# Kernel optimization log

Measured on AMD Instinct MI355X. Metric: run time of the kernel, lower is better.

The kernel has to match this reference:

```python
import jax, jax.numpy as jnp
import numpy as np
import math

EPS = 1e-5

def _bn_lrelu(x, g, b, m, v):
    # BatchNorm2d (eval, running stats) + LeakyReLU(0.01)
    inv = jax.lax.rsqrt(v + EPS)
    xn = (x - m[None, :, None, None]) * (g * inv)[None, :, None, None] + b[None, :, None, None]
    return jnp.where(xn >= 0, xn, 0.01 * xn)

def _conv3x3(x, w, b):
    # zero pad 1 on freq (dim2) and time (dim3) (pad_left state is None -> zeros), valid 3x3 conv
    x = jnp.pad(x, ((0, 0), (0, 0), (1, 1), (1, 1)))
    y = jax.lax.conv_general_dilated(x, w, (1, 1), 'VALID',
                                     dimension_numbers=('NCHW', 'OIHW', 'NCHW'))
    return y + b[None, :, None, None]

def _conv1x1(x, w, b):
    return jnp.einsum('bcft,oc->boft', x, w[:, :, 0, 0]) + b[None, :, None, None]

def _blockx3(x, g, b, m, v, w, wb):
    return _conv3x3(_bn_lrelu(x, g, b, m, v), w, wb)

def _mha(x, wqkv, bqkv, wo, bo, n_heads=4, L=64, U=128):
    # banded local attention over time, window = (L back, L fwd), chunked by U
    B, C, F, T = x.shape
    H = n_heads; D = C // H; S = 2 * L
    qkv = _conv1x1(x, wqkv, bqkv)                 # [B,3C,F,T]
    qkv = qkv.transpose(0, 2, 1, 3)               # [B,F,3C,T]
    def split(a):
        return a.reshape(B * F, H, D, T).transpose(0, 1, 3, 2)  # [BF,H,T,D]
    q = split(qkv[:, :, :C])
    k = split(qkv[:, :, C:2 * C])
    v = split(qkv[:, :, 2 * C:])
    Tkv = T + L                                   # kv padded left by L (zero state)
    nC = T // U
    pad_to = nC * U + S                           # pad kv right so every chunk window exists
    kp = jnp.pad(k, ((0, 0), (0, 0), (L, pad_to - Tkv), (0, 0)))
    vp = jnp.pad(v, ((0, 0), (0, 0), (L, pad_to - Tkv), (0, 0)))
    idx = (jnp.arange(nC) * U)[:, None] + jnp.arange(U + S)[None, :]   # [nC, U+S]
    kc = kp[:, :, idx, :]                         # [BF,H,nC,U+S,D]
    vc = vp[:, :, idx, :]
    qc = q.reshape(B * F, H, nC, U, D)
    i = jnp.arange(U)[:, None]; j = jnp.arange(U + S)[None, :]
    band = (j >= i) & (j <= i + S)                # row i sees cols i..i+S (width 1+2L)
    valid = (jnp.arange(nC)[:, None] * U + jnp.arange(U + S)[None, :]) < Tkv
    mask = (band[None, :, :] & valid[:, None, :]).astype(x.dtype)      # [nC,U,U+S]
    scores = jnp.einsum('bhcqd,bhckd->bhcqk', qc, kc) / math.sqrt(D)
    scores = scores * mask - 10000.0 * (1.0 - mask)
    p = jax.nn.softmax(scores, axis=-1)
    o = jnp.einsum('bhcqk,bhckd->bhcqd', p, vc)   # [BF,H,nC,U,D]
    o = o.reshape(B * F, H, T, D).transpose(0, 1, 3, 2).reshape(B, F, C, T).transpose(0, 2, 1, 3)
    return _conv1x1(o, wo, bo)

def setup_inputs() -> dict:
    key = jax.random.key(0)
    ks = jax.random.split(key, 40)
    d = {}
    d['x'] = jax.random.normal(ks[0], (4, 64, 64, 512), dtype=jnp.float32)
    def bn(i, c, pre):
        d[pre + '_g'] = jax.random.normal(ks[i], (c,), jnp.float32) * 0.1 + 1.0
        d[pre + '_b'] = jax.random.normal(ks[i + 1], (c,), jnp.float32) * 0.1
        d[pre + '_m'] = jax.random.normal(ks[i + 2], (c,), jnp.float32) * 0.1
        d[pre + '_v'] = jax.random.uniform(ks[i + 3], (c,), jnp.float32, 0.5, 1.5)
    def conv(i, o, c, kh, kw, pre):
        fan = c * kh * kw
        d[pre + '_w'] = jax.random.normal(ks[i], (o, c, kh, kw), jnp.float32) / math.sqrt(fan)
        d[pre + '_wb'] = jax.random.normal(ks[i + 1], (o,), jnp.float32) * 0.01
    bn(1, 64, 'bd0');  conv(5, 32, 64, 3, 3, 'bd0')
    bn(7, 96, 'bd1');  conv(11, 32, 96, 3, 3, 'bd1')
    bn(13, 128, 'bdo'); conv(17, 64, 128, 3, 3, 'bdo')
    d['qkv_w'] = jax.random.normal(ks[19], (192, 64, 1, 1), jnp.float32) / math.sqrt(64)
    d['qkv_b'] = jax.random.normal(ks[20], (192,), jnp.float32) * 0.01
    d['o_w'] = jax.random.normal(ks[21], (64, 64, 1, 1), jnp.float32) / math.sqrt(64)
    d['o_b'] = jax.random.normal(ks[22], (64,), jnp.float32) * 0.01
    bn(23, 128, 'sao'); conv(27, 64, 128, 1, 1, 'sao')
    return d

def reference(x,
              bd0_g, bd0_b, bd0_m, bd0_v, bd0_w, bd0_wb,
              bd1_g, bd1_b, bd1_m, bd1_v, bd1_w, bd1_wb,
              bdo_g, bdo_b, bdo_m, bdo_v, bdo_w, bdo_wb,
              qkv_w, qkv_b, o_w, o_b,
              sao_g, sao_b, sao_m, sao_v, sao_w, sao_wb):
    # dense conv stack: 64 -> +32 -> +32 -> 64
    a0 = _blockx3(x, bd0_g, bd0_b, bd0_m, bd0_v, bd0_w, bd0_wb)
    x1 = jnp.concatenate([x, a0], axis=1)                 # [B,96,F,T]
    a1 = _blockx3(x1, bd1_g, bd1_b, bd1_m, bd1_v, bd1_w, bd1_wb)
    x2 = jnp.concatenate([x1, a1], axis=1)                # [B,128,F,T]
    y = _blockx3(x2, bdo_g, bdo_b, bdo_m, bdo_v, bdo_w, bdo_wb)  # [B,64,F,T]
    # banded self-attention branch
    att = _mha(y, qkv_w, qkv_b, o_w, o_b)                 # [B,64,F,T]
    z = jnp.concatenate([y, att], axis=1)                 # [B,128,F,T]
    out = _conv1x1(_bn_lrelu(z, sao_g, sao_b, sao_m, sao_v), sao_w, sao_wb)
    return out
```

## Files before the change

### kernel.cpp

```cpp
#include <hip/hip_runtime.h>
#include <hip/hip_bf16.h>

typedef unsigned short u16t;
typedef __attribute__((ext_vector_type(8))) short bfrag;
typedef __attribute__((ext_vector_type(4))) float f32x4;
typedef __attribute__((ext_vector_type(8))) unsigned short uh8;

__device__ __forceinline__ float bfu(u16t u) {
    union { unsigned int i; float f; } c;
    c.i = ((unsigned int)u) << 16;
    return c.f;
}
__device__ __forceinline__ u16t fbf(float f) {
    __hip_bfloat16 h = __float2bfloat16(f);
    return *reinterpret_cast<u16t*>(&h);
}

__global__ __launch_bounds__(256) void prep_x3_k(
    const float* __restrict__ x,
    const float* __restrict__ g0, const float* __restrict__ b0,
    const float* __restrict__ m0, const float* __restrict__ v0,
    const float* __restrict__ g1, const float* __restrict__ b1,
    const float* __restrict__ m1, const float* __restrict__ v1,
    const float* __restrict__ g2, const float* __restrict__ b2,
    const float* __restrict__ m2, const float* __restrict__ v2,
    u16t* __restrict__ xn0, u16t* __restrict__ xn1, u16t* __restrict__ xn2)
{
    constexpr int F = 64, T = 512;
    __shared__ u16t su[64][74];
    __shared__ float ssc[3][64], ssh[3][64];
    const int tid = threadIdx.x;
    const int t0 = blockIdx.x * 64;
    const int f = blockIdx.y, b = blockIdx.z;

    if (tid < 64) {
        int c = tid;
        float s;
        s = g0[c] * rsqrtf(v0[c] + 1e-5f); ssc[0][c] = s; ssh[0][c] = b0[c] - m0[c] * s;
        s = g1[c] * rsqrtf(v1[c] + 1e-5f); ssc[1][c] = s; ssh[1][c] = b1[c] - m1[c] * s;
        s = g2[c] * rsqrtf(v2[c] + 1e-5f); ssc[2][c] = s; ssh[2][c] = b2[c] - m2[c] * s;
    }
#pragma unroll
    for (int p = 0; p < 16; p++) {
        int i = tid + 256 * p;
        int c = i >> 6, t = i & 63;
        su[c][t] = fbf(x[(((long)b * 64 + c) * F + f) * T + t0 + t]);
    }
    __syncthreads();
#pragma unroll
    for (int p = 0; p < 2; p++) {
        int i = tid + 256 * p;
        int t = i >> 3, c8 = i & 7;
        uh8 o0, o1, o2;
#pragma unroll
        for (int j = 0; j < 8; j++) {
            int c = c8 * 8 + j;
            float xv = bfu(su[c][t]);
            float n0 = fmaf(xv, ssc[0][c], ssh[0][c]);
            float n1 = fmaf(xv, ssc[1][c], ssh[1][c]);
            float n2 = fmaf(xv, ssc[2][c], ssh[2][c]);
            o0[j] = fbf(fmaxf(n0, 0.01f * n0));
            o1[j] = fbf(fmaxf(n1, 0.01f * n1));
            o2[j] = fbf(fmaxf(n2, 0.01f * n2));
        }
        long gi = (((long)b * F + f) * T + t0 + t) * 64 + c8 * 8;
        *(uh8*)&xn0[gi] = o0;
        *(uh8*)&xn1[gi] = o1;
        *(uh8*)&xn2[gi] = o2;
    }
}

__global__ __launch_bounds__(256) void prep_w_k(
    const float* __restrict__ w0, const float* __restrict__ w1,
    const float* __restrict__ w2, const float* __restrict__ ow,
    const float* __restrict__ sw, const float* __restrict__ qw,
    u16t* __restrict__ wp)
{
    int idx = blockIdx.x * 256 + threadIdx.x;
    if (idx >= 144384) return;
    if (idx < 119808) {
        int C_IN, C_OUT, e;
        const float* src;
        if (idx < 18432)      { C_IN = 64;  C_OUT = 32; src = w0; e = idx; }
        else if (idx < 46080) { C_IN = 96;  C_OUT = 32; src = w1; e = idx - 18432; }
        else                  { C_IN = 128; C_OUT = 64; src = w2; e = idx - 46080; }
        int NCOT = C_OUT / 16;
        int j  = e & 7;
        int l  = (e >> 3) & 63;
        int r  = e >> 9;
        int ct = r % NCOT;
        int r2 = r / NCOT;
        int kk = r2 % 9;
        int cb = r2 / 9;
        int co  = ct * 16 + (l & 15);
        int kin = cb * 32 + (l >> 4) * 8 + j;
        int kh = kk / 3, kw = kk % 3;
        wp[idx] = fbf(src[((co * C_IN + kin) * 3 + kh) * 3 + kw]);
    } else if (idx < 123904) {
        int e = idx - 119808;
        int ks = e & 31, co = (e >> 5) & 63, kb = e >> 11;
        wp[idx] = fbf(ow[co * 64 + kb * 32 + ks]);
    } else if (idx < 132096) {
        int e = idx - 123904;
        int ks = e & 31, co = (e >> 5) & 63, kb = e >> 11;
        wp[idx] = fbf(sw[co * 128 + kb * 32 + ks]);
    } else {
        int e = idx - 132096;
        int ks = e & 31, co = (e >> 5) % 192, kb = e / 6144;
        wp[idx] = fbf(qw[co * 64 + kb * 32 + ks]);
    }
}

template<int C_IN, int C_OUT, int EPI>
__global__ __launch_bounds__(256) void conv3x3_ff4_k(
    const u16t* __restrict__ s0, const u16t* __restrict__ s1,
    const u16t* __restrict__ s2,
    const u16t* __restrict__ wseg, const float* __restrict__ wb,
    const float* __restrict__ g1, const float* __restrict__ b1,
    const float* __restrict__ m1, const float* __restrict__ v1,
    const float* __restrict__ g2, const float* __restrict__ b2,
    const float* __restrict__ m2, const float* __restrict__ v2,
    int bnoff, u16t* __restrict__ dst1, u16t* __restrict__ dst2)
{
    constexpr int F = 64, T = 512, TT = 64, FF = 4;
    constexpr int NCH  = C_IN / 32;
    constexpr int NCOT = C_OUT / 16;
    constexpr int WT = 9 * NCOT * 64;
    constexpr int XT = 6 * 66 * 4;

    __shared__ __align__(16) u16t s_x[6][66][40];
    __shared__ __align__(16) u16t s_w[WT * 8];

    const int tid = threadIdx.x;
    const int t0 = blockIdx.x * TT;
    const int f0 = blockIdx.y * FF;
    const int b  = blockIdx.z;

    const int l  = tid & 63;
    const int wv = tid >> 6;
    const int lr = l & 15;
    const int lq = l >> 4;

    f32x4 acc[4][NCOT];
#pragma unroll
    for (int i = 0; i < 4; i++)
#pragma unroll
        for (int j = 0; j < NCOT; j++) acc[i][j] = (f32x4){0.f, 0.f, 0.f, 0.f};

    for (int ch = 0; ch < NCH; ch++) {
        if (ch) __syncthreads();

        for (int idx = tid; idx < XT + WT; idx += 256) {
            if (idx < XT) {
                int oct = idx & 3;
                int row = idx >> 2;
                int fr = row / 66;
                int tp = row - fr * 66;
                int fi = f0 + fr - 1;
                int tg = t0 + tp - 1;
                int gc8 = ch * 4 + oct;
                uh8 v = (uh8)0;
                if ((unsigned)fi < (unsigned)F && (unsigned)tg < (unsigned)T) {
                    const u16t* sp; int coff, cw;
                    if (C_IN == 64 || gc8 < 8) { sp = s0; coff = gc8 * 8;        cw = 64; }
                    else if (gc8 < 12)         { sp = s1; coff = (gc8 - 8) * 8;  cw = 32; }
                    else                       { sp = s2; coff = (gc8 - 12) * 8; cw = 32; }
                    v = *(const uh8*)&sp[(((long)b * F + fi) * T + tg) * cw + coff];
                }
                *(uh8*)&s_x[fr][tp][oct * 8] = v;
            } else {
                int w = idx - XT;
                *(uh8*)&s_w[w * 8] = *(const uh8*)&wseg[((long)ch * WT + w) * 8];
            }
        }
        __syncthreads();

#pragma unroll
        for (int kk = 0; kk < 9; kk++) {
            const int kh = kk / 3, kw = kk % 3;
            bfrag A[NCOT];
#pragma unroll
            for (int ct = 0; ct < NCOT; ct++)
                A[ct] = *(const bfrag*)&s_w[((kk * NCOT + ct) * 64 + l) * 8];
#pragma unroll
            for (int ts = 0; ts < 4; ts++) {
                bfrag B = *(const bfrag*)&s_x[wv + kh][ts * 16 + lr + kw][lq * 8];
#pragma unroll
                for (int ct = 0; ct < NCOT; ct++)
                    acc[ts][ct] = __builtin_amdgcn_mfma_f32_16x16x32_bf16(
                        A[ct], B, acc[ts][ct], 0, 0, 0);
            }
        }
    }

    const int f = f0 + wv;
#pragma unroll
    for (int ct = 0; ct < NCOT; ct++) {
        const int co0 = ct * 16 + lq * 4;
        float4 bs = *(const float4*)&wb[co0];
        float sc1[4], sh1[4], sc2[4], sh2[4];
        if (EPI >= 1) {
#pragma unroll
            for (int j = 0; j < 4; j++) {
                int c = bnoff + co0 + j;
                float s = g1[c] * rsqrtf(v1[c] + 1e-5f);
                sc1[j] = s; sh1[j] = b1[c] - m1[c] * s;
            }
        }
        if (EPI == 2) {
#pragma unroll
            for (int j = 0; j < 4; j++) {
                int c = bnoff + co0 + j;
                float s = g2[c] * rsqrtf(v2[c] + 1e-5f);
                sc2[j] = s; sh2[j] = b2[c] - m2[c] * s;
            }
        }
#pragma unroll
        for (int ts = 0; ts < 4; ts++) {
            const int t = t0 + ts * 16 + lr;
            long ob = (((long)b * F + f) * T + t) * C_OUT + co0;
            float a[4];
            a[0] = acc[ts][ct][0] + bs.x;
            a[1] = acc[ts][ct][1] + bs.y;
            a[2] = acc[ts][ct][2] + bs.z;
            a[3] = acc[ts][ct][3] + bs.w;
            if (EPI == 0) {
                ushort4 pk;
                pk.x = fbf(a[0]); pk.y = fbf(a[1]);
                pk.z = fbf(a[2]); pk.w = fbf(a[3]);
                *(ushort4*)&dst1[ob] = pk;
            } else {
                ushort4 p1;
#pragma unroll
                for (int j = 0; j < 4; j++) {
                    float n = fmaf(a[j], sc1[j], sh1[j]);
                    ((u16t*)&p1)[j] = fbf(fmaxf(n, 0.01f * n));
                }
                *(ushort4*)&dst1[ob] = p1;
                if (EPI == 2) {
                    ushort4 p2;
#pragma unroll
                    for (int j = 0; j < 4; j++) {
                        float n = fmaf(a[j], sc2[j], sh2[j]);
                        ((u16t*)&p2)[j] = fbf(fmaxf(n, 0.01f * n));
                    }
                    *(ushort4*)&dst2[ob] = p2;
                }
            }
        }
    }
}

__global__ __launch_bounds__(256) void qkv_mfma_k(
    const u16t* __restrict__ ybf, const u16t* __restrict__ wq,
    const float* __restrict__ qbias,
    u16t* __restrict__ q_t, u16t* __restrict__ k_t, u16t* __restrict__ v_t)
{
    constexpr int F = 64, T = 512;
    __shared__ __align__(16) u16t s_y[64][72];
    const int tid = threadIdx.x;
    const int t0 = blockIdx.x * 64;
    const int f = blockIdx.y, b = blockIdx.z;
    const long bf = (long)b * F + f;

    for (int i = tid; i < 512; i += 256) {
        int tt = i >> 3, c0 = (i & 7) * 8;
        *(uh8*)&s_y[tt][c0] = *(const uh8*)&ybf[(bf * T + t0 + tt) * 64 + c0];
    }
    __syncthreads();

    const int l = tid & 63, wv = tid >> 6;
    const int lr = l & 15, lq = l >> 4;
    const int tb = wv * 16 + lr;

    bfrag B0 = *(const bfrag*)&s_y[tb][lq * 8];
    bfrag B1 = *(const bfrag*)&s_y[tb][32 + lq * 8];

    f32x4 acc[12];
#pragma unroll
    for (int i = 0; i < 12; i++) acc[i] = (f32x4){0.f, 0.f, 0.f, 0.f};
#pragma unroll
    for (int ct = 0; ct < 12; ct++) {
        bfrag A0 = *(const bfrag*)&wq[(ct * 16 + lr) * 32 + lq * 8];
        acc[ct] = __builtin_amdgcn_mfma_f32_16x16x32_bf16(A0, B0, acc[ct], 0, 0, 0);
    }
#pragma unroll
    for (int ct = 0; ct < 12; ct++) {
        bfrag A1 = *(const bfrag*)&wq[(192 + ct * 16 + lr) * 32 + lq * 8];
        acc[ct] = __builtin_amdgcn_mfma_f32_16x16x32_bf16(A1, B1, acc[ct], 0, 0, 0);
    }

    const int t = t0 + tb;
#pragma unroll
    for (int ct = 0; ct < 12; ct++) {
        int co0 = ct * 16 + lq * 4;
        float4 bi = *(const float4*)&qbias[co0];
        float a0 = acc[ct][0] + bi.x, a1 = acc[ct][1] + bi.y;
        float a2 = acc[ct][2] + bi.z, a3 = acc[ct][3] + bi.w;
        if (co0 < 64) {
            ushort4 pk;
            pk.x = fbf(a0 * 0.25f); pk.y = fbf(a1 * 0.25f);
            pk.z = fbf(a2 * 0.25f); pk.w = fbf(a3 * 0.25f);
            *(ushort4*)&q_t[(bf * T + t) * 64 + co0] = pk;
        } else if (co0 < 128) {
            int hh = (co0 - 64) >> 4, d0 = (co0 - 64) & 15;
            ushort4 pk;
            pk.x = fbf(a0); pk.y = fbf(a1); pk.z = fbf(a2); pk.w = fbf(a3);
            *(ushort4*)&k_t[((bf * 4 + hh) * T + t) * 16 + d0] = pk;
        } else {
            int hh = (co0 - 128) >> 4, d0 = (co0 - 128) & 15;
            long vb = (bf * 4 + hh) * 16;
            v_t[(vb + d0 + 0) * T + t] = fbf(a0);
            v_t[(vb + d0 + 1) * T + t] = fbf(a1);
            v_t[(vb + d0 + 2) * T + t] = fbf(a2);
            v_t[(vb + d0 + 3) * T + t] = fbf(a3);
        }
    }
}

__global__ __launch_bounds__(256) void attn_mfma_k(
    const u16t* __restrict__ qt, const u16t* __restrict__ kt_,
    const u16t* __restrict__ vt, u16t* __restrict__ ob)
{
    constexpr int T = 512, F = 64;
    const int qc = blockIdx.x & 7;
    const int h  = blockIdx.x >> 3;
    const int f = blockIdx.y, b = blockIdx.z;
    const int qb0 = qc * 64;
    const int tid = threadIdx.x;
    const long bf = (long)b * F + f;
    const long kvb = bf * 4 + h;

    __shared__ __align__(16) u16t s_k[192][24];
    __shared__ __align__(16) u16t s_v[16][216];
    __shared__ __align__(16) u16t s_p[4][16][168];
    __shared__ __align__(16) u16t s_zero[8];

    if (tid < 8) s_zero[tid] = 0;

    for (int idx = tid; idx < 384; idx += 256) {
        int kk = idx >> 1, hv = idx & 1;
        int p = qb0 - 64 + kk;
        uh8 v = (uh8)0;
        if ((unsigned)p < (unsigned)T)
            v = *(const uh8*)&kt_[(kvb * T + p) * 16 + hv * 8];
        *(uh8*)&s_k[kk][hv * 8] = v;
    }
    for (int idx = tid; idx < 432; idx += 256) {
        int d = idx / 27, c8 = idx % 27;
        int kk0 = c8 * 8;
        int p0 = qb0 - 64 + kk0;
        uh8 v = (uh8)0;
        if (p0 >= 0 && p0 + 7 < T) {
            v = *(const uh8*)&vt[(kvb * 16 + d) * T + p0];
        } else {
#pragma unroll
            for (int j = 0; j < 8; j++) {
                int p = p0 + j;
                v[j] = ((unsigned)p < (unsigned)T)
                     ? vt[(kvb * 16 + d) * T + p] : (u16t)0;
            }
        }
        *(uh8*)&s_v[d][kk0] = v;
    }
    __syncthreads();

    const int l  = tid & 63;
    const int wv = tid >> 6;
    const int lr = l & 15;
    const int lq = l >> 4;
    const int qt0 = qb0 + wv * 16;

    bfrag Bq = (bfrag)0;
    if (lq < 2)
        Bq = *(const bfrag*)&qt[(bf * T + qt0 + lr) * 64 + h * 16 + lq * 8];

    f32x4 sf[9];
#pragma unroll
    for (int kti = 0; kti < 9; kti++) {
        const u16t* ap = (lq < 2) ? &s_k[wv * 16 + kti * 16 + lr][lq * 8]
                                  : &s_zero[0];
        bfrag A = *(const bfrag*)ap;
        sf[kti] = __builtin_amdgcn_mfma_f32_16x16x32_bf16(
            A, Bq, (f32x4){0.f, 0.f, 0.f, 0.f}, 0, 0, 0);
    }

    float m = -3.0e38f;
#pragma unroll
    for (int kti = 0; kti < 9; kti++) {
#pragma unroll
        for (int j = 0; j < 4; j++) {
            int rk = kti * 16 + lq * 4 + j;
            int dq = rk - lr;
            int p  = qt0 - 64 + rk;
            float s = sf[kti][j];
            s = (dq >= 0 && dq <= 128 && p < T) ? s : -1.0e30f;
            sf[kti][j] = s;
            m = fmaxf(m, s);
        }
    }
    m = fmaxf(m, __shfl_xor(m, 16));
    m = fmaxf(m, __shfl_xor(m, 32));

    float lsum = 0.f;
#pragma unroll
    for (int kti = 0; kti < 9; kti++) {
#pragma unroll
        for (int j = 0; j < 4; j++) {
            float e = __expf(sf[kti][j] - m);
            sf[kti][j] = e;
            lsum += e;
        }
    }
    lsum += __shfl_xor(lsum, 16);
    lsum += __shfl_xor(lsum, 32);

#pragma unroll
    for (int kti = 0; kti < 9; kti++) {
        ushort4 pk;
        pk.x = fbf(sf[kti][0]); pk.y = fbf(sf[kti][1]);
        pk.z = fbf(sf[kti][2]); pk.w = fbf(sf[kti][3]);
        *(ushort4*)&s_p[wv][lr][kti * 16 + lq * 4] = pk;
    }
    {
        ushort4 z; z.x = 0; z.y = 0; z.z = 0; z.w = 0;
        *(ushort4*)&s_p[wv][lr][144 + lq * 4] = z;
    }
    __syncthreads();

    f32x4 oa = (f32x4){0.f, 0.f, 0.f, 0.f};
#pragma unroll
    for (int kc = 0; kc < 5; kc++) {
        bfrag Av = *(const bfrag*)&s_v[lr][wv * 16 + kc * 32 + lq * 8];
        bfrag Bp = *(const bfrag*)&s_p[wv][lr][kc * 32 + lq * 8];
        oa = __builtin_amdgcn_mfma_f32_16x16x32_bf16(Av, Bp, oa, 0, 0, 0);
    }
    const float inv = 1.0f / lsum;
    ushort4 ov;
    ov.x = fbf(oa[0] * inv); ov.y = fbf(oa[1] * inv);
    ov.z = fbf(oa[2] * inv); ov.w = fbf(oa[3] * inv);
    *(ushort4*)&ob[(bf * T + qt0 + lr) * 64 + h * 16 + lq * 4] = ov;
}

__global__ __launch_bounds__(256) void final_mfma_k(
    const u16t* __restrict__ ob, const u16t* __restrict__ yb,
    const u16t* __restrict__ wo, const float* __restrict__ obias,
    const float* __restrict__ sg, const float* __restrict__ sb,
    const float* __restrict__ sm, const float* __restrict__ sv,
    const u16t* __restrict__ wsao, const float* __restrict__ swb,
    float* __restrict__ out)
{
    constexpr int F = 64, T = 512, TT = 64, P = 72;
    __shared__ __align__(16) u16t s_ob[64][P];
    __shared__ __align__(16) u16t s_y2[64][P];
    __shared__ __align__(16) u16t s_att[64][P];
    __shared__ float s_sc[128], s_sh[128];

    const int tid = threadIdx.x;
    const int t0 = blockIdx.x * TT;
    const int f = blockIdx.y, b = blockIdx.z;

    if (tid < 128) {
        float sc = sg[tid] * rsqrtf(sv[tid] + 1e-5f);
        s_sc[tid] = sc;
        s_sh[tid] = sb[tid] - sm[tid] * sc;
    }
    __syncthreads();

    for (int i = tid; i < 512; i += 256) {
        int tt = i >> 3, c0 = (i & 7) * 8;
        long gi = (((long)b * F + f) * T + t0 + tt) * 64 + c0;
        *(uh8*)&s_ob[tt][c0] = *(const uh8*)&ob[gi];
        uh8 raw = *(const uh8*)&yb[gi];
        uh8 v;
#pragma unroll
        for (int j = 0; j < 8; j++) {
            float xv = bfu(raw[j]);
            float xn = fmaf(xv, s_sc[c0 + j], s_sh[c0 + j]);
            v[j] = fbf(fmaxf(xn, 0.01f * xn));
        }
        *(uh8*)&s_y2[tt][c0] = v;
    }
    __syncthreads();

    const int l  = tid & 63;
    const int wv = tid >> 6;
    const int lr = l & 15;
    const int lq = l >> 4;
    const int tbase = wv * 16 + lr;
    const int cbase = lq * 8;

    f32x4 acc1[4];
#pragma unroll
    for (int i = 0; i < 4; i++) acc1[i] = (f32x4){0.f, 0.f, 0.f, 0.f};
#pragma unroll
    for (int kb = 0; kb < 2; kb++) {
        bfrag B = *(const bfrag*)&s_ob[tbase][kb * 32 + cbase];
#pragma unroll
        for (int ct = 0; ct < 4; ct++) {
            bfrag A = *(const bfrag*)&wo[(kb * 64 + ct * 16 + lr) * 32 + lq * 8];
            acc1[ct] = __builtin_amdgcn_mfma_f32_16x16x32_bf16(A, B, acc1[ct], 0, 0, 0);
        }
    }
#pragma unroll
    for (int ct = 0; ct < 4; ct++) {
        int co = ct * 16 + lq * 4;
        float4 bi = *(const float4*)&obias[co];
#pragma unroll
        for (int j = 0; j < 4; j++) {
            float a = acc1[ct][j] + ((j == 0) ? bi.x : (j == 1) ? bi.y : (j == 2) ? bi.z : bi.w);
            int cg = 64 + co + j;
            float xn = fmaf(a, s_sc[cg], s_sh[cg]);
            s_att[tbase][co + j] = fbf(fmaxf(xn, 0.01f * xn));
        }
    }
    __syncthreads();

    f32x4 acc2[4];
#pragma unroll
    for (int i = 0; i < 4; i++) acc2[i] = (f32x4){0.f, 0.f, 0.f, 0.f};
#pragma unroll
    for (int kb = 0; kb < 4; kb++) {
        bfrag B = (kb < 2) ? *(const bfrag*)&s_y2[tbase][kb * 32 + cbase]
                           : *(const bfrag*)&s_att[tbase][(kb - 2) * 32 + cbase];
#pragma unroll
        for (int ct = 0; ct < 4; ct++) {
            bfrag A = *(const bfrag*)&wsao[(kb * 64 + ct * 16 + lr) * 32 + lq * 8];
            acc2[ct] = __builtin_amdgcn_mfma_f32_16x16x32_bf16(A, B, acc2[ct], 0, 0, 0);
        }
    }
    const int t = t0 + wv * 16 + lr;
#pragma unroll
    for (int ct = 0; ct < 4; ct++) {
        int co0 = ct * 16 + lq * 4;
        float4 bs = *(const float4*)&swb[co0];
#pragma unroll
        for (int j = 0; j < 4; j++) {
            float bv = (j == 0) ? bs.x : (j == 1) ? bs.y : (j == 2) ? bs.z : bs.w;
            out[(((long)b * 64 + co0 + j) * F + f) * T + t] = acc2[ct][j] + bv;
        }
    }
}

extern "C" void kernel_launch(void* const* d_in, const int* in_sizes, int n_in,
                              void* d_out, int out_size, void* d_ws, size_t ws_size,
                              hipStream_t stream)
{
    (void)in_sizes; (void)n_in; (void)out_size; (void)ws_size;

    const float* x      = (const float*)d_in[0];
    const float* bd0_g  = (const float*)d_in[1];
    const float* bd0_b  = (const float*)d_in[2];
    const float* bd0_m  = (const float*)d_in[3];
    const float* bd0_v  = (const float*)d_in[4];
    const float* bd0_w  = (const float*)d_in[5];
    const float* bd0_wb = (const float*)d_in[6];
    const float* bd1_g  = (const float*)d_in[7];
    const float* bd1_b  = (const float*)d_in[8];
    const float* bd1_m  = (const float*)d_in[9];
    const float* bd1_v  = (const float*)d_in[10];
    const float* bd1_w  = (const float*)d_in[11];
    const float* bd1_wb = (const float*)d_in[12];
    const float* bdo_g  = (const float*)d_in[13];
    const float* bdo_b  = (const float*)d_in[14];
    const float* bdo_m  = (const float*)d_in[15];
    const float* bdo_v  = (const float*)d_in[16];
    const float* bdo_w  = (const float*)d_in[17];
    const float* bdo_wb = (const float*)d_in[18];
    const float* qkv_w  = (const float*)d_in[19];
    const float* qkv_b  = (const float*)d_in[20];
    const float* o_w    = (const float*)d_in[21];
    const float* o_b    = (const float*)d_in[22];
    const float* sao_g  = (const float*)d_in[23];
    const float* sao_b  = (const float*)d_in[24];
    const float* sao_m  = (const float*)d_in[25];
    const float* sao_v  = (const float*)d_in[26];
    const float* sao_w  = (const float*)d_in[27];
    const float* sao_wb = (const float*)d_in[28];

    char* ws = (char*)d_ws;
    u16t* xn0  = (u16t*)(ws);
    u16t* xn1  = (u16t*)(ws + 16777216);
    u16t* xn2  = (u16t*)(ws + 33554432);
    u16t* a0n1 = (u16t*)(ws + 50331648);
    u16t* a0n2 = (u16t*)(ws + 58720256);
    u16t* a1n2 = (u16t*)(ws + 67108864);
    u16t* ybf  = xn0;
    u16t* q_t  = xn1;
    u16t* k_t  = xn2;
    u16t* v_t  = a0n1;
    u16t* obf  = q_t;
    u16t* wpk  = (u16t*)(ws + 75497472);

    dim3 blk(256);
    dim3 gprep(8, 64, 4);
    dim3 gconv(8, 16, 4);

    hipLaunchKernelGGL(prep_x3_k, gprep, blk, 0, stream, x,
        bd0_g, bd0_b, bd0_m, bd0_v, bd1_g, bd1_b, bd1_m, bd1_v,
        bdo_g, bdo_b, bdo_m, bdo_v, xn0, xn1, xn2);
    hipLaunchKernelGGL(prep_w_k, dim3(564), blk, 0, stream,
        bd0_w, bd1_w, bdo_w, o_w, sao_w, qkv_w, wpk);
    hipLaunchKernelGGL((conv3x3_ff4_k<64, 32, 2>), gconv, blk, 0, stream,
        xn0, nullptr, nullptr, wpk, bd0_wb,
        bd1_g, bd1_b, bd1_m, bd1_v, bdo_g, bdo_b, bdo_m, bdo_v,
        64, a0n1, a0n2);
    hipLaunchKernelGGL((conv3x3_ff4_k<96, 32, 1>), gconv, blk, 0, stream,
        xn1, a0n1, nullptr, wpk + 18432, bd1_wb,
        bdo_g, bdo_b, bdo_m, bdo_v, nullptr, nullptr, nullptr, nullptr,
        96, a1n2, nullptr);
    hipLaunchKernelGGL((conv3x3_ff4_k<128, 64, 0>), gconv, blk, 0, stream,
        xn2, a0n2, a1n2, wpk + 46080, bdo_wb,
        nullptr, nullptr, nullptr, nullptr, nullptr, nullptr, nullptr, nullptr,
        0, ybf, nullptr);
    hipLaunchKernelGGL(qkv_mfma_k, gprep, blk, 0, stream,
        ybf, wpk + 132096, qkv_b, q_t, k_t, v_t);
    hipLaunchKernelGGL(attn_mfma_k, dim3(32, 64, 4), blk, 0, stream,
        q_t, k_t, v_t, obf);
    hipLaunchKernelGGL(final_mfma_k, gprep, blk, 0, stream,
        obf, ybf, wpk + 119808, o_b, sao_g, sao_b, sao_m, sao_v,
        wpk + 123904, sao_wb, (float*)d_out);
}
```

Measured before the change: 182.4 us.

## Load attention K/V fragments straight to registers, use exp2 and simplify interior masking

The banded attention kernel no longer stages K and V tiles in shared memory behind a block barrier. Each wave now loads its own MFMA K and V fragments directly from global memory into registers and zeroes out-of-range fragments only for the first and last query chunks. The log2(e) factor is folded into the Q scale in the projection kernel so the softmax can use exp2. The full band/bounds mask is replaced by a cheaper diagonal-edge mask for interior chunks. In exchange, edge chunks issue loads outside the valid rows (later discarded), which can read past buffer bounds, and waves no longer share staged K/V.

```diff
diff --git a/kernel.cpp b/kernel.cpp
--- a/kernel.cpp
+++ b/kernel.cpp
@@ -290,6 +290,7 @@
         acc[ct] = __builtin_amdgcn_mfma_f32_16x16x32_bf16(A1, B1, acc[ct], 0, 0, 0);
     }
 
+    const float QS = 0.25f * 1.44269504088896f;
     const int t = t0 + tb;
 #pragma unroll
     for (int ct = 0; ct < 12; ct++) {
@@ -299,8 +300,8 @@
         float a2 = acc[ct][2] + bi.z, a3 = acc[ct][3] + bi.w;
         if (co0 < 64) {
             ushort4 pk;
-            pk.x = fbf(a0 * 0.25f); pk.y = fbf(a1 * 0.25f);
-            pk.z = fbf(a2 * 0.25f); pk.w = fbf(a3 * 0.25f);
+            pk.x = fbf(a0 * QS); pk.y = fbf(a1 * QS);
+            pk.z = fbf(a2 * QS); pk.w = fbf(a3 * QS);
             *(ushort4*)&q_t[(bf * T + t) * 64 + co0] = pk;
         } else if (co0 < 128) {
             int hh = (co0 - 64) >> 4, d0 = (co0 - 64) & 15;
@@ -331,39 +332,7 @@
     const long bf = (long)b * F + f;
     const long kvb = bf * 4 + h;
 
-    __shared__ __align__(16) u16t s_k[192][24];
-    __shared__ __align__(16) u16t s_v[16][216];
     __shared__ __align__(16) u16t s_p[4][16][168];
-    __shared__ __align__(16) u16t s_zero[8];
-
-    if (tid < 8) s_zero[tid] = 0;
-
-    for (int idx = tid; idx < 384; idx += 256) {
-        int kk = idx >> 1, hv = idx & 1;
-        int p = qb0 - 64 + kk;
-        uh8 v = (uh8)0;
-        if ((unsigned)p < (unsigned)T)
-            v = *(const uh8*)&kt_[(kvb * T + p) * 16 + hv * 8];
-        *(uh8*)&s_k[kk][hv * 8] = v;
-    }
-    for (int idx = tid; idx < 432; idx += 256) {
-        int d = idx / 27, c8 = idx % 27;
-        int kk0 = c8 * 8;
-        int p0 = qb0 - 64 + kk0;
-        uh8 v = (uh8)0;
-        if (p0 >= 0 && p0 + 7 < T) {
-            v = *(const uh8*)&vt[(kvb * 16 + d) * T + p0];
-        } else {
-#pragma unroll
-            for (int j = 0; j < 8; j++) {
-                int p = p0 + j;
-                v[j] = ((unsigned)p < (unsigned)T)
-                     ? vt[(kvb * 16 + d) * T + p] : (u16t)0;
-            }
-        }
-        *(uh8*)&s_v[d][kk0] = v;
-    }
-    __syncthreads();
 
     const int l  = tid & 63;
     const int wv = tid >> 6;
@@ -375,43 +344,79 @@
     if (lq < 2)
         Bq = *(const bfrag*)&qt[(bf * T + qt0 + lr) * 64 + h * 16 + lq * 8];
 
+    bfrag Kf[9];
+    const int pK0 = qt0 - 64 + lr;
+#pragma unroll
+    for (int kti = 0; kti < 9; kti++) {
+        if (lq < 2)
+            Kf[kti] = *(const bfrag*)&kt_[(kvb * T + pK0 + kti * 16) * 16 + lq * 8];
+        else
+            Kf[kti] = (bfrag)0;
+    }
+    bfrag Vf[5];
+    const int pV0 = qb0 - 64 + wv * 16 + lq * 8;
+#pragma unroll
+    for (int kc = 0; kc < 5; kc++)
+        Vf[kc] = *(const bfrag*)&vt[(kvb * 16 + lr) * T + pV0 + kc * 32];
+
+    if (qc == 0) {
+#pragma unroll
+        for (int kti = 0; kti < 9; kti++)
+            if (pK0 + kti * 16 < 0) Kf[kti] = (bfrag)0;
+#pragma unroll
+        for (int kc = 0; kc < 5; kc++)
+            if (pV0 + kc * 32 < 0) Vf[kc] = (bfrag)0;
+    }
+    if (qc == 7) {
+#pragma unroll
+        for (int kc = 0; kc < 5; kc++)
+            if (pV0 + kc * 32 >= T) Vf[kc] = (bfrag)0;
+    }
+
     f32x4 sf[9];
 #pragma unroll
-    for (int kti = 0; kti < 9; kti++) {
-        const u16t* ap = (lq < 2) ? &s_k[wv * 16 + kti * 16 + lr][lq * 8]
-                                  : &s_zero[0];
-        bfrag A = *(const bfrag*)ap;
+    for (int kti = 0; kti < 9; kti++)
         sf[kti] = __builtin_amdgcn_mfma_f32_16x16x32_bf16(
-            A, Bq, (f32x4){0.f, 0.f, 0.f, 0.f}, 0, 0, 0);
-    }
+            Kf[kti], Bq, (f32x4){0.f, 0.f, 0.f, 0.f}, 0, 0, 0);
 
     float m = -3.0e38f;
-#pragma unroll
-    for (int kti = 0; kti < 9; kti++) {
+    if (qc == 7) {
+#pragma unroll
+        for (int kti = 0; kti < 9; kti++)
+#pragma unroll
+            for (int j = 0; j < 4; j++) {
+                int rk = kti * 16 + lq * 4 + j;
+                int dq = rk - lr;
+                int p  = qt0 - 64 + rk;
+                float s = sf[kti][j];
+                s = (dq >= 0 && dq <= 128 && p < T) ? s : -1.0e30f;
+                sf[kti][j] = s;
+                m = fmaxf(m, s);
+            }
+    } else {
 #pragma unroll
         for (int j = 0; j < 4; j++) {
-            int rk = kti * 16 + lq * 4 + j;
-            int dq = rk - lr;
-            int p  = qt0 - 64 + rk;
-            float s = sf[kti][j];
-            s = (dq >= 0 && dq <= 128 && p < T) ? s : -1.0e30f;
-            sf[kti][j] = s;
-            m = fmaxf(m, s);
-        }
+            int rk0 = lq * 4 + j;
+            if (rk0 < lr)      sf[0][j] = -1.0e30f;
+            if (rk0 > lr)      sf[8][j] = -1.0e30f;
+        }
+#pragma unroll
+        for (int kti = 0; kti < 9; kti++)
+#pragma unroll
+            for (int j = 0; j < 4; j++) m = fmaxf(m, sf[kti][j]);
     }
     m = fmaxf(m, __shfl_xor(m, 16));
     m = fmaxf(m, __shfl_xor(m, 32));
 
     float lsum = 0.f;
 #pragma unroll
-    for (int kti = 0; kti < 9; kti++) {
+    for (int kti = 0; kti < 9; kti++)
 #pragma unroll
         for (int j = 0; j < 4; j++) {
-            float e = __expf(sf[kti][j] - m);
+            float e = exp2f(sf[kti][j] - m);
             sf[kti][j] = e;
             lsum += e;
         }
-    }
     lsum += __shfl_xor(lsum, 16);
     lsum += __shfl_xor(lsum, 32);
 
@@ -431,9 +436,8 @@
     f32x4 oa = (f32x4){0.f, 0.f, 0.f, 0.f};
 #pragma unroll
     for (int kc = 0; kc < 5; kc++) {
-        bfrag Av = *(const bfrag*)&s_v[lr][wv * 16 + kc * 32 + lq * 8];
         bfrag Bp = *(const bfrag*)&s_p[wv][lr][kc * 32 + lq * 8];
-        oa = __builtin_amdgcn_mfma_f32_16x16x32_bf16(Av, Bp, oa, 0, 0, 0);
+        oa = __builtin_amdgcn_mfma_f32_16x16x32_bf16(Vf[kc], Bp, oa, 0, 0, 0);
     }
     const float inv = 1.0f / lsum;
     ushort4 ov;
```

Result: faster. 177.2 us (-2.9%).
